# Kernel optimization log

Measured on AMD Instinct MI355X. Metric: run time of the kernel, lower is better.

The kernel has to match this reference:

```python
import jax, jax.numpy as jnp
import numpy as np

N, E, F_IN, HEADS, OUT_PER_HEAD = 50000, 1600000, 128, 4, 32
NEG_SLOPE = 0.2  # LeakyReLU slope used by standard GATConv


def setup_inputs() -> dict:
    key = jax.random.key(0)
    ks = jax.random.split(key, 7)
    x = jax.random.normal(ks[0], (N, F_IN), dtype=jnp.float32)
    edge_src = jax.random.randint(ks[1], (E,), 0, N, dtype=jnp.int64)
    edge_dst = jax.random.randint(ks[2], (E,), 0, N, dtype=jnp.int64)
    W = jax.random.normal(ks[3], (F_IN, HEADS * OUT_PER_HEAD), dtype=jnp.float32) / np.float32(np.sqrt(F_IN))
    a_src = jax.random.normal(ks[4], (HEADS, OUT_PER_HEAD), dtype=jnp.float32) * 0.1
    a_dst = jax.random.normal(ks[5], (HEADS, OUT_PER_HEAD), dtype=jnp.float32) * 0.1
    bias = jnp.zeros((HEADS * OUT_PER_HEAD,), dtype=jnp.float32)
    return {"x": x, "W": W, "a_src": a_src, "a_dst": a_dst, "bias": bias,
            "edge_src": edge_src, "edge_dst": edge_dst}


def reference(x, W, a_src, a_dst, bias, edge_src, edge_dst):
    # GATConv with concat=True over a static edge list (the faithful
    # static-shape form of tf.where(adj>0.5) -> gather -> GAT -> scatter).
    n = x.shape[0]
    H, D = a_src.shape
    h = (x @ W).reshape(n, H, D)                      # [N,H,D] projected features
    # per-node attention logits for source / destination roles
    e_s = jnp.einsum('nhd,hd->nh', h, a_src)          # [N,H]
    e_d = jnp.einsum('nhd,hd->nh', h, a_dst)          # [N,H]
    # per-edge logits with LeakyReLU
    e = jax.nn.leaky_relu(e_s[edge_src] + e_d[edge_dst], NEG_SLOPE)  # [E,H]
    # numerically stable softmax over incoming edges of each destination node
    m = jax.ops.segment_max(e, edge_dst, num_segments=n)             # [N,H]
    m = jnp.where(jnp.isfinite(m), m, 0.0)
    alpha = jnp.exp(e - m[edge_dst])                                 # [E,H]
    denom = jax.ops.segment_sum(alpha, edge_dst, num_segments=n)     # [N,H]
    alpha = alpha / jnp.where(denom > 0, denom, 1.0)[edge_dst]
    # weighted aggregation of source features onto destinations
    msgs = alpha[:, :, None] * h[edge_src]                           # [E,H,D]
    out = jax.ops.segment_sum(msgs, edge_dst, num_segments=n)        # [N,H,D]
    return out.reshape(n, H * D) + bias
```

## Files before the change

kernel.cpp:

```cpp
#include <hip/hip_runtime.h>
#include <math.h>

#define NEG_SLOPE 0.2f
#define XROW 136
#define BSHIFT 4
#define BNODES 16
#define NBUCK_MAX 3200
#define CAP 768
#define NHB 256

typedef __attribute__((ext_vector_type(8))) short short8;
typedef __attribute__((ext_vector_type(4))) float floatx4;

__device__ __forceinline__ unsigned short f2bf(float f) {
    unsigned int u = __float_as_uint(f);
    u += 0x7fffu + ((u >> 16) & 1u);
    return (unsigned short)(u >> 16);
}
__device__ __forceinline__ float bf2f(unsigned short b) {
    return __uint_as_float(((unsigned int)b) << 16);
}
__device__ __forceinline__ float u2fl(unsigned int u) {
    return __uint_as_float(u << 16);
}
__device__ __forceinline__ float u2fh(unsigned int u) {
    return __uint_as_float(u & 0xffff0000u);
}

__device__ __forceinline__ void fma8(float* a, int o, float wt, const uint4& hv) {
    a[o + 0] = fmaf(wt, u2fl(hv.x), a[o + 0]);
    a[o + 1] = fmaf(wt, u2fh(hv.x), a[o + 1]);
    a[o + 2] = fmaf(wt, u2fl(hv.y), a[o + 2]);
    a[o + 3] = fmaf(wt, u2fh(hv.y), a[o + 3]);
    a[o + 4] = fmaf(wt, u2fl(hv.z), a[o + 4]);
    a[o + 5] = fmaf(wt, u2fh(hv.z), a[o + 5]);
    a[o + 6] = fmaf(wt, u2fl(hv.w), a[o + 6]);
    a[o + 7] = fmaf(wt, u2fh(hv.w), a[o + 7]);
}

__device__ __forceinline__ int eph_of(int e) {
    return (((e + NHB - 1) / NHB) + 3) & ~3;
}

__global__ __launch_bounds__(256) void hist_prep_kernel(
    const float* __restrict__ W, unsigned short* __restrict__ WThi,
    unsigned short* __restrict__ WTlo, const int* __restrict__ dst,
    int* __restrict__ C, int e, int nbuck)
{
    __shared__ int hist[NBUCK_MAX];
    const int t = threadIdx.x;
    const int idx = blockIdx.x * 256 + t;
    if (idx < 16384) {
        const int j = idx >> 7, k = idx & 127;
        const float w = W[k * 128 + j];
        const unsigned short hi = f2bf(w);
        WThi[idx] = hi;
        WTlo[idx] = f2bf(w - bf2f(hi));
    }
    for (int b = t; b < nbuck; b += 256) hist[b] = 0;
    __syncthreads();
    const int eph = eph_of(e);
    const int base = blockIdx.x * eph;
    const int m = min(e - base, eph);
    if (m > 0) {
        const int m4 = m >> 2;
        for (int j = t; j < m4; j += 256) {
            const int4 d4 = *(const int4*)(dst + base + j * 4);
            atomicAdd(&hist[d4.x >> BSHIFT], 1);
            atomicAdd(&hist[d4.y >> BSHIFT], 1);
            atomicAdd(&hist[d4.z >> BSHIFT], 1);
            atomicAdd(&hist[d4.w >> BSHIFT], 1);
        }
        for (int j = m4 * 4 + t; j < m; j += 256)
            atomicAdd(&hist[dst[base + j] >> BSHIFT], 1);
    }
    __syncthreads();
    for (int b = t; b < nbuck; b += 256)
        C[(size_t)blockIdx.x * nbuck + b] = hist[b];
}

__global__ __launch_bounds__(256) void scan_kernel(
    int* __restrict__ C, int* __restrict__ btot, int nbuck)
{
    const int b = blockIdx.x * 256 + threadIdx.x;
    if (b >= nbuck) return;
    int off = 0;
    #pragma unroll 4
    for (int k = 0; k < NHB; ++k) {
        const int v = C[(size_t)k * nbuck + b];
        C[(size_t)k * nbuck + b] = off;
        off += v;
    }
    btot[b] = off;
}

__global__ __launch_bounds__(256) void scatter_kernel(
    const int* __restrict__ src, const int* __restrict__ dst,
    const int* __restrict__ C, int* __restrict__ ebuf, int e, int nbuck)
{
    __shared__ int cur[NBUCK_MAX];
    const int t = threadIdx.x;
    for (int b = t; b < nbuck; b += 256)
        cur[b] = b * CAP + C[(size_t)blockIdx.x * nbuck + b];
    __syncthreads();
    const int eph = eph_of(e);
    const int base = blockIdx.x * eph;
    const int m = min(e - base, eph);
    if (m <= 0) return;
    const int m4 = m >> 2;
    for (int j = t; j < m4; j += 256) {
        const int i0 = base + j * 4;
        const int4 s4 = *(const int4*)(src + i0);
        const int4 d4 = *(const int4*)(dst + i0);
        int bk, pos;
        bk = d4.x >> BSHIFT; pos = atomicAdd(&cur[bk], 1);
        if (pos < bk * CAP + CAP) ebuf[pos] = s4.x | ((d4.x & 15) << 16);
        bk = d4.y >> BSHIFT; pos = atomicAdd(&cur[bk], 1);
        if (pos < bk * CAP + CAP) ebuf[pos] = s4.y | ((d4.y & 15) << 16);
        bk = d4.z >> BSHIFT; pos = atomicAdd(&cur[bk], 1);
        if (pos < bk * CAP + CAP) ebuf[pos] = s4.z | ((d4.z & 15) << 16);
        bk = d4.w >> BSHIFT; pos = atomicAdd(&cur[bk], 1);
        if (pos < bk * CAP + CAP) ebuf[pos] = s4.w | ((d4.w & 15) << 16);
    }
    for (int j = m4 * 4 + t; j < m; j += 256) {
        const int d = dst[base + j];
        const int bk = d >> BSHIFT;
        const int pos = atomicAdd(&cur[bk], 1);
        if (pos < bk * CAP + CAP) ebuf[pos] = src[base + j] | ((d & 15) << 16);
    }
}

__global__ __launch_bounds__(256) void mfma_gemm_kernel(
    const float* __restrict__ x, const unsigned short* __restrict__ WThi,
    const unsigned short* __restrict__ WTlo, const float* __restrict__ a_src,
    const float* __restrict__ a_dst, unsigned short* __restrict__ hb,
    float* __restrict__ es, float* __restrict__ ed, int n)
{
    __shared__ unsigned short Xhi[32 * XROW];
    __shared__ unsigned short Xlo[32 * XROW];
    const int t = threadIdx.x;
    const int wv = t >> 6, lane = t & 63;
    const int l16 = lane & 15, quad = lane >> 4;
    const int node_base = blockIdx.x * 32;

    short8 bh[4][2], bl[4][2];
    #pragma unroll
    for (int c = 0; c < 4; ++c) {
        #pragma unroll
        for (int u = 0; u < 2; ++u) {
            const int j = (wv * 2 + u) * 16 + l16;
            const int ko = c * 32 + quad * 8;
            bh[c][u] = *(const short8*)&WThi[j * 128 + ko];
            bl[c][u] = *(const short8*)&WTlo[j * 128 + ko];
        }
    }

    for (int i = t; i < 1024; i += 256) {
        const int nd = i >> 5;
        const int k4 = i & 31;
        float4 xv = make_float4(0.f, 0.f, 0.f, 0.f);
        if (node_base + nd < n)
            xv = ((const float4*)(x + (size_t)(node_base + nd) * 128))[k4];
        const unsigned short h0 = f2bf(xv.x), h1 = f2bf(xv.y),
                             h2 = f2bf(xv.z), h3 = f2bf(xv.w);
        const unsigned short l0 = f2bf(xv.x - bf2f(h0)), l1 = f2bf(xv.y - bf2f(h1)),
                             l2 = f2bf(xv.z - bf2f(h2)), l3 = f2bf(xv.w - bf2f(h3));
        *(ushort4*)&Xhi[nd * XROW + k4 * 4] = make_ushort4(h0, h1, h2, h3);
        *(ushort4*)&Xlo[nd * XROW + k4 * 4] = make_ushort4(l0, l1, l2, l3);
    }
    __syncthreads();

    floatx4 acc[2][2] = {};
    #pragma unroll
    for (int c = 0; c < 4; ++c) {
        const int ko = c * 32 + quad * 8;
        short8 ah[2], al[2];
        #pragma unroll
        for (int r = 0; r < 2; ++r) {
            ah[r] = *(const short8*)&Xhi[(r * 16 + l16) * XROW + ko];
            al[r] = *(const short8*)&Xlo[(r * 16 + l16) * XROW + ko];
        }
        #pragma unroll
        for (int r = 0; r < 2; ++r)
        #pragma unroll
        for (int u = 0; u < 2; ++u) {
            acc[r][u] = __builtin_amdgcn_mfma_f32_16x16x32_bf16(ah[r], bl[c][u], acc[r][u], 0, 0, 0);
            acc[r][u] = __builtin_amdgcn_mfma_f32_16x16x32_bf16(al[r], bh[c][u], acc[r][u], 0, 0, 0);
            acc[r][u] = __builtin_amdgcn_mfma_f32_16x16x32_bf16(ah[r], bh[c][u], acc[r][u], 0, 0, 0);
        }
    }

    float asv[2], adv[2];
    #pragma unroll
    for (int u = 0; u < 2; ++u) {
        const int feat = (wv * 2 + u) * 16 + l16;
        asv[u] = a_src[feat];
        adv[u] = a_dst[feat];
    }
    #pragma unroll
    for (int r = 0; r < 2; ++r) {
        #pragma unroll
        for (int u = 0; u < 2; ++u) {
            const int feat = (wv * 2 + u) * 16 + l16;
            #pragma unroll
            for (int g = 0; g < 4; ++g) {
                const int node = node_base + r * 16 + quad * 4 + g;
                if (node < n)
                    hb[(size_t)node * 128 + feat] = f2bf(acc[r][u][g]);
            }
        }
        #pragma unroll
        for (int g = 0; g < 4; ++g) {
            float ps = acc[r][0][g] * asv[0] + acc[r][1][g] * asv[1];
            float pd = acc[r][0][g] * adv[0] + acc[r][1][g] * adv[1];
            #pragma unroll
            for (int o = 8; o >= 1; o >>= 1) {
                ps += __shfl_xor(ps, o);
                pd += __shfl_xor(pd, o);
            }
            const int node = node_base + r * 16 + quad * 4 + g;
            if (l16 == 0 && node < n) {
                es[node * 4 + wv] = ps;
                ed[node * 4 + wv] = pd;
            }
        }
    }
}

__global__ __launch_bounds__(256) void sort_agg_kernel(
    const unsigned short* __restrict__ hb, const float* __restrict__ es,
    const float* __restrict__ ed, const float* __restrict__ bias,
    const int* __restrict__ btot, const int* __restrict__ ebuf,
    float* __restrict__ out, int n)
{
    __shared__ unsigned short esort[CAP];
    __shared__ int hist[BNODES], hexcl[BNODES], cur[BNODES];
    const int b = blockIdx.x;
    const int t = threadIdx.x;
    const int lane = t & 63;
    const int wv = t >> 6;
    const int l8 = lane & 7;
    const int oct = lane >> 3;
    const int f0 = l8 * 16;
    const int hh = l8 >> 1;

    const int start = b * CAP;
    const int end = start + min(btot[b], CAP);

    if (t < BNODES) hist[t] = 0;
    __syncthreads();
    for (int i = start + t; i < end; i += 256)
        atomicAdd(&hist[(ebuf[i] >> 16) & (BNODES - 1)], 1);
    __syncthreads();
    if (wv == 0) {
        const int v = (lane < BNODES) ? hist[lane] : 0;
        int incl = v;
        #pragma unroll
        for (int o = 1; o < BNODES; o <<= 1) {
            const int tt = __shfl_up(incl, o);
            if (lane >= o) incl += tt;
        }
        if (lane < BNODES) { hexcl[lane] = incl - v; cur[lane] = incl - v; }
    }
    __syncthreads();
    for (int i = start + t; i < end; i += 256) {
        const int v = ebuf[i];
        const int pos = atomicAdd(&cur[(v >> 16) & (BNODES - 1)], 1);
        if (pos < CAP) esort[pos] = (unsigned short)(v & 0xFFFF);
    }
    __syncthreads();

    for (int j = 0; j < 4; ++j) {
        const int nd = wv * 4 + j;
        const int node = b * BNODES + nd;
        if (node >= n) break;
        const int off = hexcl[nd];
        const int deg = hist[nd];
        const float edh = ed[(size_t)node * 4 + hh];

        float a[16];
        #pragma unroll
        for (int k = 0; k < 16; ++k) a[k] = 0.f;
        float wsum = 0.f;

        for (int c0 = 0; c0 < deg; c0 += 16) {
            const int ci0 = c0 + oct;
            const int ci1 = ci0 + 8;
            const int dm = deg - 1;
            const int s0 = esort[min(off + min(ci0, dm), CAP - 1)];
            const int s1 = esort[min(off + min(ci1, dm), CAP - 1)];
            const float e0 = es[(size_t)s0 * 4 + hh];
            const float e1 = es[(size_t)s1 * 4 + hh];
            const uint4 hA0 = *(const uint4*)&hb[(size_t)s0 * 128 + f0];
            const uint4 hB0 = *(const uint4*)&hb[(size_t)s0 * 128 + f0 + 8];
            const uint4 hA1 = *(const uint4*)&hb[(size_t)s1 * 128 + f0];
            const uint4 hB1 = *(const uint4*)&hb[(size_t)s1 * 128 + f0 + 8];
            float lg0 = e0 + edh; lg0 = lg0 > 0.f ? lg0 : NEG_SLOPE * lg0;
            float lg1 = e1 + edh; lg1 = lg1 > 0.f ? lg1 : NEG_SLOPE * lg1;
            const float w0 = (ci0 < deg) ? __expf(lg0) : 0.f;
            const float w1 = (ci1 < deg) ? __expf(lg1) : 0.f;
            fma8(a, 0, w0, hA0); fma8(a, 8, w0, hB0);
            fma8(a, 0, w1, hA1); fma8(a, 8, w1, hB1);
            wsum += w0 + w1;
        }
        #pragma unroll
        for (int o = 8; o <= 32; o <<= 1) {
            #pragma unroll
            for (int k = 0; k < 16; ++k) a[k] += __shfl_xor(a[k], o);
            wsum += __shfl_xor(wsum, o);
        }
        if (oct == 0) {
            const float inv = 1.f / ((wsum > 0.f) ? wsum : 1.f);
            #pragma unroll
            for (int q = 0; q < 4; ++q) {
                const float4 bq = *(const float4*)(bias + f0 + q * 4);
                float4 o4;
                o4.x = a[q * 4 + 0] * inv + bq.x;
                o4.y = a[q * 4 + 1] * inv + bq.y;
                o4.z = a[q * 4 + 2] * inv + bq.z;
                o4.w = a[q * 4 + 3] * inv + bq.w;
                *(float4*)(out + (size_t)node * 128 + f0 + q * 4) = o4;
            }
        }
    }
}

extern "C" void kernel_launch(void* const* d_in, const int* in_sizes, int n_in,
                              void* d_out, int out_size, void* d_ws, size_t ws_size,
                              hipStream_t stream)
{
    const float* x      = (const float*)d_in[0];
    const float* W      = (const float*)d_in[1];
    const float* a_src  = (const float*)d_in[2];
    const float* a_dst  = (const float*)d_in[3];
    const float* bias   = (const float*)d_in[4];
    const int*   e_src  = (const int*)d_in[5];
    const int*   e_dst  = (const int*)d_in[6];
    float* out = (float*)d_out;

    const int n = in_sizes[0] / 128;
    const int e = in_sizes[5];
    const int nbuck = (n + BNODES - 1) >> BSHIFT;

    char* ws = (char*)d_ws;
    size_t o = 0;
    auto alloc = [&](size_t bytes) { void* p = ws + o; o += (bytes + 255) & ~(size_t)255; return p; };
    unsigned short* hb   = (unsigned short*)alloc((size_t)n * 128 * sizeof(unsigned short));
    unsigned short* WThi = (unsigned short*)alloc(128 * 128 * sizeof(unsigned short));
    unsigned short* WTlo = (unsigned short*)alloc(128 * 128 * sizeof(unsigned short));
    float* es      = (float*)alloc((size_t)n * 4 * sizeof(float));
    float* ed      = (float*)alloc((size_t)n * 4 * sizeof(float));
    int* C         = (int*)alloc((size_t)NHB * nbuck * sizeof(int));
    int* btot      = (int*)alloc((size_t)nbuck * sizeof(int));
    int* ebuf      = (int*)alloc((size_t)nbuck * CAP * sizeof(int));
    (void)ws_size; (void)n_in; (void)out_size;

    hist_prep_kernel<<<NHB, 256, 0, stream>>>(W, WThi, WTlo, e_dst, C, e, nbuck);
    scan_kernel<<<(nbuck + 255) / 256, 256, 0, stream>>>(C, btot, nbuck);
    scatter_kernel<<<NHB, 256, 0, stream>>>(e_src, e_dst, C, ebuf, e, nbuck);
    mfma_gemm_kernel<<<(n + 31) / 32, 256, 0, stream>>>(x, WThi, WTlo, a_src, a_dst,
                                                        hb, es, ed, n);
    sort_agg_kernel<<<nbuck, 256, 0, stream>>>(hb, es, ed, bias, btot, ebuf, out, n);
}
```

Baseline: 232.3 us.

## Fuse histogram, scan and scatter into one cooperative kernel with grid syncs

Merges the three edge-bucketing kernels (histogram, per-bucket scan, scatter) into a single cooperative launch of 256 blocks that uses grid-wide syncs in place of kernel boundaries. This removes two launches and their gaps, and lets the shared-memory counter array be reused. In the GEMM kernel, all x loads are issued into registers before conversion, and a min-blocks launch bound is added to raise memory-level parallelism. Grid syncs carry their own cost, and the scan phase runs on only a few of the 256 blocks while the rest wait.

After: 343.9 us. +48.0%, slower.

```diff
diff --git a/kernel.cpp b/kernel.cpp
--- a/kernel.cpp
+++ b/kernel.cpp
@@ -1,4 +1,5 @@
 #include <hip/hip_runtime.h>
+#include <hip/hip_cooperative_groups.h>
 #include <math.h>
 
 #define NEG_SLOPE 0.2f
@@ -8,6 +9,8 @@
 #define NBUCK_MAX 3200
 #define CAP 768
 #define NHB 256
+
+namespace cg = cooperative_groups;
 
 typedef __attribute__((ext_vector_type(8))) short short8;
 typedef __attribute__((ext_vector_type(4))) float floatx4;
@@ -42,95 +45,93 @@
     return (((e + NHB - 1) / NHB) + 3) & ~3;
 }
 
-__global__ __launch_bounds__(256) void hist_prep_kernel(
+__global__ __launch_bounds__(256) void edge_pipeline_kernel(
     const float* __restrict__ W, unsigned short* __restrict__ WThi,
-    unsigned short* __restrict__ WTlo, const int* __restrict__ dst,
-    int* __restrict__ C, int e, int nbuck)
+    unsigned short* __restrict__ WTlo, const int* __restrict__ src,
+    const int* __restrict__ dst, int* __restrict__ C,
+    int* __restrict__ btot, int* __restrict__ ebuf, int e, int nbuck)
 {
-    __shared__ int hist[NBUCK_MAX];
+    __shared__ int cnt[NBUCK_MAX];
+    cg::grid_group grid = cg::this_grid();
     const int t = threadIdx.x;
-    const int idx = blockIdx.x * 256 + t;
-    if (idx < 16384) {
-        const int j = idx >> 7, k = idx & 127;
+    const int blk = blockIdx.x;
+    const int gid = blk * 256 + t;
+
+    if (gid < 16384) {
+        const int j = gid >> 7, k = gid & 127;
         const float w = W[k * 128 + j];
         const unsigned short hi = f2bf(w);
-        WThi[idx] = hi;
-        WTlo[idx] = f2bf(w - bf2f(hi));
-    }
-    for (int b = t; b < nbuck; b += 256) hist[b] = 0;
+        WThi[gid] = hi;
+        WTlo[gid] = f2bf(w - bf2f(hi));
+    }
+
+    for (int b = t; b < nbuck; b += 256) cnt[b] = 0;
     __syncthreads();
     const int eph = eph_of(e);
-    const int base = blockIdx.x * eph;
+    const int base = blk * eph;
     const int m = min(e - base, eph);
     if (m > 0) {
         const int m4 = m >> 2;
         for (int j = t; j < m4; j += 256) {
             const int4 d4 = *(const int4*)(dst + base + j * 4);
-            atomicAdd(&hist[d4.x >> BSHIFT], 1);
-            atomicAdd(&hist[d4.y >> BSHIFT], 1);
-            atomicAdd(&hist[d4.z >> BSHIFT], 1);
-            atomicAdd(&hist[d4.w >> BSHIFT], 1);
+            atomicAdd(&cnt[d4.x >> BSHIFT], 1);
+            atomicAdd(&cnt[d4.y >> BSHIFT], 1);
+            atomicAdd(&cnt[d4.z >> BSHIFT], 1);
+            atomicAdd(&cnt[d4.w >> BSHIFT], 1);
         }
         for (int j = m4 * 4 + t; j < m; j += 256)
-            atomicAdd(&hist[dst[base + j] >> BSHIFT], 1);
+            atomicAdd(&cnt[dst[base + j] >> BSHIFT], 1);
     }
     __syncthreads();
     for (int b = t; b < nbuck; b += 256)
-        C[(size_t)blockIdx.x * nbuck + b] = hist[b];
-}
-
-__global__ __launch_bounds__(256) void scan_kernel(
-    int* __restrict__ C, int* __restrict__ btot, int nbuck)
-{
-    const int b = blockIdx.x * 256 + threadIdx.x;
-    if (b >= nbuck) return;
-    int off = 0;
-    #pragma unroll 4
-    for (int k = 0; k < NHB; ++k) {
-        const int v = C[(size_t)k * nbuck + b];
-        C[(size_t)k * nbuck + b] = off;
-        off += v;
-    }
-    btot[b] = off;
-}
-
-__global__ __launch_bounds__(256) void scatter_kernel(
-    const int* __restrict__ src, const int* __restrict__ dst,
-    const int* __restrict__ C, int* __restrict__ ebuf, int e, int nbuck)
-{
-    __shared__ int cur[NBUCK_MAX];
-    const int t = threadIdx.x;
+        C[(size_t)blk * nbuck + b] = cnt[b];
+
+    __threadfence();
+    grid.sync();
+
+    if (gid < nbuck) {
+        int off = 0;
+        #pragma unroll 4
+        for (int k = 0; k < NHB; ++k) {
+            const int v = C[(size_t)k * nbuck + gid];
+            C[(size_t)k * nbuck + gid] = off;
+            off += v;
+        }
+        btot[gid] = off;
+    }
+
+    __threadfence();
+    grid.sync();
+
     for (int b = t; b < nbuck; b += 256)
-        cur[b] = b * CAP + C[(size_t)blockIdx.x * nbuck + b];
-    __syncthreads();
-    const int eph = eph_of(e);
-    const int base = blockIdx.x * eph;
-    const int m = min(e - base, eph);
-    if (m <= 0) return;
-    const int m4 = m >> 2;
-    for (int j = t; j < m4; j += 256) {
-        const int i0 = base + j * 4;
-        const int4 s4 = *(const int4*)(src + i0);
-        const int4 d4 = *(const int4*)(dst + i0);
-        int bk, pos;
-        bk = d4.x >> BSHIFT; pos = atomicAdd(&cur[bk], 1);
-        if (pos < bk * CAP + CAP) ebuf[pos] = s4.x | ((d4.x & 15) << 16);
-        bk = d4.y >> BSHIFT; pos = atomicAdd(&cur[bk], 1);
-        if (pos < bk * CAP + CAP) ebuf[pos] = s4.y | ((d4.y & 15) << 16);
-        bk = d4.z >> BSHIFT; pos = atomicAdd(&cur[bk], 1);
-        if (pos < bk * CAP + CAP) ebuf[pos] = s4.z | ((d4.z & 15) << 16);
-        bk = d4.w >> BSHIFT; pos = atomicAdd(&cur[bk], 1);
-        if (pos < bk * CAP + CAP) ebuf[pos] = s4.w | ((d4.w & 15) << 16);
-    }
-    for (int j = m4 * 4 + t; j < m; j += 256) {
-        const int d = dst[base + j];
-        const int bk = d >> BSHIFT;
-        const int pos = atomicAdd(&cur[bk], 1);
-        if (pos < bk * CAP + CAP) ebuf[pos] = src[base + j] | ((d & 15) << 16);
-    }
-}
-
-__global__ __launch_bounds__(256) void mfma_gemm_kernel(
+        cnt[b] = b * CAP + C[(size_t)blk * nbuck + b];
+    __syncthreads();
+    if (m > 0) {
+        const int m4 = m >> 2;
+        for (int j = t; j < m4; j += 256) {
+            const int i0 = base + j * 4;
+            const int4 s4 = *(const int4*)(src + i0);
+            const int4 d4 = *(const int4*)(dst + i0);
+            int bk, pos;
+            bk = d4.x >> BSHIFT; pos = atomicAdd(&cnt[bk], 1);
+            if (pos < bk * CAP + CAP) ebuf[pos] = s4.x | ((d4.x & 15) << 16);
+            bk = d4.y >> BSHIFT; pos = atomicAdd(&cnt[bk], 1);
+            if (pos < bk * CAP + CAP) ebuf[pos] = s4.y | ((d4.y & 15) << 16);
+            bk = d4.z >> BSHIFT; pos = atomicAdd(&cnt[bk], 1);
+            if (pos < bk * CAP + CAP) ebuf[pos] = s4.z | ((d4.z & 15) << 16);
+            bk = d4.w >> BSHIFT; pos = atomicAdd(&cnt[bk], 1);
+            if (pos < bk * CAP + CAP) ebuf[pos] = s4.w | ((d4.w & 15) << 16);
+        }
+        for (int j = m4 * 4 + t; j < m; j += 256) {
+            const int d = dst[base + j];
+            const int bk = d >> BSHIFT;
+            const int pos = atomicAdd(&cnt[bk], 1);
+            if (pos < bk * CAP + CAP) ebuf[pos] = src[base + j] | ((d & 15) << 16);
+        }
+    }
+}
+
+__global__ __launch_bounds__(256, 4) void mfma_gemm_kernel(
     const float* __restrict__ x, const unsigned short* __restrict__ WThi,
     const unsigned short* __restrict__ WTlo, const float* __restrict__ a_src,
     const float* __restrict__ a_dst, unsigned short* __restrict__ hb,
@@ -143,6 +144,29 @@
     const int l16 = lane & 15, quad = lane >> 4;
     const int node_base = blockIdx.x * 32;
 
+    float4 xv[4];
+    #pragma unroll
+    for (int it = 0; it < 4; ++it) {
+        const int i = t + it * 256;
+        const int nd = i >> 5, k4 = i & 31;
+        float4 v = make_float4(0.f, 0.f, 0.f, 0.f);
+        if (node_base + nd < n)
+            v = ((const float4*)(x + (size_t)(node_base + nd) * 128))[k4];
+        xv[it] = v;
+    }
+    #pragma unroll
+    for (int it = 0; it < 4; ++it) {
+        const int i = t + it * 256;
+        const int nd = i >> 5, k4 = i & 31;
+        const float4 v = xv[it];
+        const unsigned short h0 = f2bf(v.x), h1 = f2bf(v.y),
+                             h2 = f2bf(v.z), h3 = f2bf(v.w);
+        const unsigned short l0 = f2bf(v.x - bf2f(h0)), l1 = f2bf(v.y - bf2f(h1)),
+                             l2 = f2bf(v.z - bf2f(h2)), l3 = f2bf(v.w - bf2f(h3));
+        *(ushort4*)&Xhi[nd * XROW + k4 * 4] = make_ushort4(h0, h1, h2, h3);
+        *(ushort4*)&Xlo[nd * XROW + k4 * 4] = make_ushort4(l0, l1, l2, l3);
+    }
+
     short8 bh[4][2], bl[4][2];
     #pragma unroll
     for (int c = 0; c < 4; ++c) {
@@ -153,20 +177,6 @@
             bh[c][u] = *(const short8*)&WThi[j * 128 + ko];
             bl[c][u] = *(const short8*)&WTlo[j * 128 + ko];
         }
-    }
-
-    for (int i = t; i < 1024; i += 256) {
-        const int nd = i >> 5;
-        const int k4 = i & 31;
-        float4 xv = make_float4(0.f, 0.f, 0.f, 0.f);
-        if (node_base + nd < n)
-            xv = ((const float4*)(x + (size_t)(node_base + nd) * 128))[k4];
-        const unsigned short h0 = f2bf(xv.x), h1 = f2bf(xv.y),
-                             h2 = f2bf(xv.z), h3 = f2bf(xv.w);
-        const unsigned short l0 = f2bf(xv.x - bf2f(h0)), l1 = f2bf(xv.y - bf2f(h1)),
-                             l2 = f2bf(xv.z - bf2f(h2)), l3 = f2bf(xv.w - bf2f(h3));
-        *(ushort4*)&Xhi[nd * XROW + k4 * 4] = make_ushort4(h0, h1, h2, h3);
-        *(ushort4*)&Xlo[nd * XROW + k4 * 4] = make_ushort4(l0, l1, l2, l3);
     }
     __syncthreads();
 
@@ -339,8 +349,8 @@
     float* out = (float*)d_out;
 
     const int n = in_sizes[0] / 128;
-    const int e = in_sizes[5];
-    const int nbuck = (n + BNODES - 1) >> BSHIFT;
+    int e = in_sizes[5];
+    int nbuck = (n + BNODES - 1) >> BSHIFT;
 
     char* ws = (char*)d_ws;
     size_t o = 0;
@@ -355,9 +365,11 @@
     int* ebuf      = (int*)alloc((size_t)nbuck * CAP * sizeof(int));
     (void)ws_size; (void)n_in; (void)out_size;
 
-    hist_prep_kernel<<<NHB, 256, 0, stream>>>(W, WThi, WTlo, e_dst, C, e, nbuck);
-    scan_kernel<<<(nbuck + 255) / 256, 256, 0, stream>>>(C, btot, nbuck);
-    scatter_kernel<<<NHB, 256, 0, stream>>>(e_src, e_dst, C, ebuf, e, nbuck);
+    void* args[] = {(void*)&W, (void*)&WThi, (void*)&WTlo, (void*)&e_src,
+                    (void*)&e_dst, (void*)&C, (void*)&btot, (void*)&ebuf,
+                    (void*)&e, (void*)&nbuck};
+    hipLaunchCooperativeKernel((const void*)edge_pipeline_kernel,
+                               dim3(NHB), dim3(256), args, 0, stream);
     mfma_gemm_kernel<<<(n + 31) / 32, 256, 0, stream>>>(x, WThi, WTlo, a_src, a_dst,
                                                         hb, es, ed, n);
     sort_agg_kernel<<<nbuck, 256, 0, stream>>>(hb, es, ed, bias, btot, ebuf, out, n);
```
